# Performance work log

Hardware: AMD Instinct MI355X
Metric: run time of the kernel (lower is better)

The kernel has to match this reference:

```python
import jax, jax.numpy as jnp
import numpy as np

NUM_HEADS = 16


def setup_inputs() -> dict:
    rng = jax.random.key(0)
    ks = jax.random.split(rng, 11)
    T, B, E = 1024, 4, 1024
    s = E ** -0.5  # weight init scale
    return {
        "query": jax.random.normal(ks[0], (T, B, E), jnp.float32),
        "key": jax.random.normal(ks[1], (T, B, E), jnp.float32),
        "value": jax.random.normal(ks[2], (T, B, E), jnp.float32),
        "q_proj_weight": jax.random.normal(ks[3], (E, E), jnp.float32) * s,
        "k_proj_weight1": jax.random.normal(ks[4], (E, E), jnp.float32) * s,
        "k_proj_weight2": jax.random.normal(ks[5], (E, E), jnp.float32) * s,
        "v_proj_weight": jax.random.normal(ks[6], (E, E), jnp.float32) * s,
        "in_proj_bias": jax.random.normal(ks[7], (4 * E,), jnp.float32) * 0.02,
        "out_proj_weight": jax.random.normal(ks[8], (E, E), jnp.float32) * s,
        "out_proj_bias": jax.random.normal(ks[9], (E,), jnp.float32) * 0.02,
        "pi": jax.random.uniform(ks[10], (2, NUM_HEADS), jnp.float32, 0.3, 0.7),
    }


def reference(query, key, value, q_proj_weight, k_proj_weight1, k_proj_weight2,
              v_proj_weight, in_proj_bias, out_proj_weight, out_proj_bias, pi):
    T, Bz, E = query.shape
    H = NUM_HEADS
    hd = E // H
    scaling = hd ** -0.5

    b_q, b_k1, b_k2, b_v = jnp.split(in_proj_bias, 4)
    q = query @ q_proj_weight.T + b_q
    k1 = key @ k_proj_weight1.T + b_k1
    k2 = key @ k_proj_weight2.T + b_k2
    v = value @ v_proj_weight.T + b_v

    def heads(x):  # (S, B, E) -> (B*H, S, hd)
        S = x.shape[0]
        return x.reshape(S, Bz * H, hd).transpose(1, 0, 2)

    q, k1, k2, v = heads(q), heads(k1), heads(k2), heads(v)

    def sqdist(a, b):  # (B*H, Nt, hd), (B*H, Ns, hd) -> (B*H, Nt, Ns)
        a2 = jnp.sum(a * a, axis=-1)
        b2 = jnp.sum(b * b, axis=-1)
        ab = jnp.einsum('btd,bsd->bts', a, b)
        return a2[:, :, None] + b2[:, None, :] - 2.0 * ab

    e1 = jnp.exp(-scaling / 2.0 * sqdist(q, k1))
    e2 = jnp.exp(-3.0 * scaling / 2.0 * sqdist(q, k2))

    pi1 = jnp.clip(jnp.abs(pi[0]), 1e-6, 2.0)  # (H,)
    pi2 = jnp.clip(jnp.abs(pi[1]), 1e-6, 2.0)

    Nt, Ns = e1.shape[1], e1.shape[2]
    attn = (e1.reshape(Bz, H, Nt, Ns) * pi1[None, :, None, None]
            + e2.reshape(Bz, H, Nt, Ns) * pi2[None, :, None, None])
    attn = attn.reshape(Bz * H, Nt, Ns)
    attn = attn / (jnp.sum(attn, axis=-1, keepdims=True) + 1e-6)

    out = jnp.einsum('bts,bsd->btd', attn, v)        # (B*H, Nt, hd)
    out = out.transpose(1, 0, 2).reshape(T, Bz, E)   # (T, B, E)
    return out @ out_proj_weight.T + out_proj_bias
```

## Files before the change

kernel.cpp:

```cpp
#include <hip/hip_runtime.h>
#include <hip/hip_bf16.h>

#define T_DIM 1024
#define B_DIM 4
#define E_DIM 1024
#define H_DIM 16
#define HD    64
#define M_DIM (T_DIM * B_DIM)

typedef __hip_bfloat16 bf16;
typedef __bf16 bf16x8 __attribute__((ext_vector_type(8)));
typedef __bf16 bf16x4 __attribute__((ext_vector_type(4)));
typedef __bf16 bf16x2 __attribute__((ext_vector_type(2)));
typedef float  f32x4  __attribute__((ext_vector_type(4)));

#define P4S ((size_t)M_DIM * E_DIM)
#define P1S ((size_t)E_DIM * E_DIM)

__global__ __launch_bounds__(256) void cvt_all(
    const float* __restrict__ q, const float* __restrict__ k,
    const float* __restrict__ v, const float* __restrict__ w0,
    const float* __restrict__ w1, const float* __restrict__ w2,
    const float* __restrict__ w3, const float* __restrict__ w4,
    __bf16* __restrict__ dst)
{
  size_t i = ((size_t)blockIdx.x * 256 + threadIdx.x) * 8;
  const float* src;
  size_t off;
  if (i < P4S)            { src = q; off = i; }
  else if (i < 2 * P4S)   { src = k; off = i - P4S; }
  else if (i < 3 * P4S)   { src = v; off = i - 2 * P4S; }
  else {
    size_t j = i - 3 * P4S;
    int wsel = (int)(j >> 20);
    off = j & (P1S - 1);
    const float* ws[5] = {w0, w1, w2, w3, w4};
    src = ws[wsel];
  }
  float4 a = *(const float4*)(src + off);
  float4 b = *(const float4*)(src + off + 4);
  bf16x8 o;
  o[0] = (__bf16)a.x; o[1] = (__bf16)a.y; o[2] = (__bf16)a.z; o[3] = (__bf16)a.w;
  o[4] = (__bf16)b.x; o[5] = (__bf16)b.y; o[6] = (__bf16)b.z; o[7] = (__bf16)b.w;
  *(bf16x8*)(dst + i) = o;
}

__device__ __forceinline__ void load_lds16(const __bf16* g, __bf16* l) {
  __builtin_amdgcn_global_load_lds(
      (__attribute__((address_space(1))) void*)(void*)g,
      (__attribute__((address_space(3))) void*)l, 16, 0, 0);
}

__device__ __forceinline__ void stage_half(
    int H, const __bf16* __restrict__ X, const __bf16* __restrict__ W,
    int bm, int bn, __bf16* As, __bf16* Bs, int tid)
{
  if (H >= 64) return;
  const int T  = H >> 2;
  const int h  = H & 3;
  const int rh = (h & 1) * 128;
  const __bf16* src = (h < 2) ? X : W;
  const int rbase   = (h < 2) ? bm : bn;
  __bf16* lb = ((h < 2) ? As : Bs) + (T & 1) * 16384;
#pragma unroll
  for (int li = 0; li < 2; ++li) {
    int r  = rh + li * 64 + (tid >> 3);
    int gc = (tid & 7) ^ (r & 7);
    load_lds16(src + (size_t)(rbase + r) * E_DIM + T * 64 + gc * 8,
               lb + (rh + li * 64) * 64 + tid * 8);
  }
}

#define RD(base, row, c) \
  (*(const bf16x8*)((base) + (row) * 64 + ((((c) ^ ((row) & 7))) << 3)))

__global__ __launch_bounds__(512, 2) void proj_gemm4(
    const __bf16* __restrict__ xbase, const __bf16* __restrict__ wbase,
    const float* __restrict__ bin, __bf16* __restrict__ cbase)
{
  __shared__ __bf16 lds[65536];
  __bf16* As = lds;
  __bf16* Bs = lds + 32768;

  const int z = blockIdx.z;
  const __bf16* X = xbase + ((z == 0) ? 0 : (z == 3) ? 2 * P4S : P4S);
  const __bf16* W = wbase + (size_t)z * P1S;
  const float* bias = bin + z * E_DIM;
  __bf16* C = cbase + (size_t)z * P4S;

  const int bm = blockIdx.x * 256;
  const int bn = blockIdx.y * 256;

  const int tid  = threadIdx.x;
  const int lane = tid & 63;
  const int w    = tid >> 6;
  const int wm   = w >> 2;
  const int wn   = w & 3;
  const int mrow = lane & 15, quad = lane >> 4;

  f32x4 acc[8][4];
#pragma unroll
  for (int m = 0; m < 8; ++m)
#pragma unroll
    for (int n = 0; n < 4; ++n) acc[m][n] = (f32x4)0.0f;

#pragma unroll
  for (int H = 0; H < 5; ++H) stage_half(H, X, W, bm, bn, As, Bs, tid);
  asm volatile("s_waitcnt vmcnt(2)" ::: "memory");
  __builtin_amdgcn_s_barrier();

  bf16x8 af[4][2];
  bf16x8 bq[4][2];

#pragma unroll 2
  for (int t = 0; t < 16; ++t) {
    const __bf16* Ab = As + (t & 1) * 16384;
    const __bf16* Bb = Bs + (t & 1) * 16384;

#pragma unroll
    for (int n = 0; n < 2; ++n)
#pragma unroll
      for (int kk = 0; kk < 2; ++kk)
        bq[n][kk] = RD(Bb, wn * 64 + n * 16 + mrow, kk * 4 + quad);
#pragma unroll
    for (int m = 0; m < 4; ++m)
#pragma unroll
      for (int kk = 0; kk < 2; ++kk)
        af[m][kk] = RD(Ab, wm * 128 + m * 16 + mrow, kk * 4 + quad);
    stage_half(4 * t + 5, X, W, bm, bn, As, Bs, tid);
    __builtin_amdgcn_s_barrier();
    asm volatile("s_waitcnt lgkmcnt(0)" ::: "memory");
    __builtin_amdgcn_s_setprio(1);
#pragma unroll
    for (int kk = 0; kk < 2; ++kk)
#pragma unroll
      for (int n = 0; n < 2; ++n)
#pragma unroll
        for (int m = 0; m < 4; ++m)
          acc[m][n] = __builtin_amdgcn_mfma_f32_16x16x32_bf16(
              af[m][kk], bq[n][kk], acc[m][n], 0, 0, 0);
    __builtin_amdgcn_s_setprio(0);
    __builtin_amdgcn_s_barrier();

#pragma unroll
    for (int n = 2; n < 4; ++n)
#pragma unroll
      for (int kk = 0; kk < 2; ++kk)
        bq[n][kk] = RD(Bb, wn * 64 + n * 16 + mrow, kk * 4 + quad);
    stage_half(4 * t + 6, X, W, bm, bn, As, Bs, tid);
    __builtin_amdgcn_s_barrier();
    asm volatile("s_waitcnt lgkmcnt(0)" ::: "memory");
    __builtin_amdgcn_s_setprio(1);
#pragma unroll
    for (int kk = 0; kk < 2; ++kk)
#pragma unroll
      for (int n = 2; n < 4; ++n)
#pragma unroll
        for (int m = 0; m < 4; ++m)
          acc[m][n] = __builtin_amdgcn_mfma_f32_16x16x32_bf16(
              af[m][kk], bq[n][kk], acc[m][n], 0, 0, 0);
    __builtin_amdgcn_s_setprio(0);
    __builtin_amdgcn_s_barrier();

#pragma unroll
    for (int m = 0; m < 4; ++m)
#pragma unroll
      for (int kk = 0; kk < 2; ++kk)
        af[m][kk] = RD(Ab, wm * 128 + 64 + m * 16 + mrow, kk * 4 + quad);
    stage_half(4 * t + 7, X, W, bm, bn, As, Bs, tid);
    __builtin_amdgcn_s_barrier();
    asm volatile("s_waitcnt lgkmcnt(0)" ::: "memory");
    __builtin_amdgcn_s_setprio(1);
#pragma unroll
    for (int kk = 0; kk < 2; ++kk)
#pragma unroll
      for (int n = 0; n < 2; ++n)
#pragma unroll
        for (int m = 0; m < 4; ++m)
          acc[4 + m][n] = __builtin_amdgcn_mfma_f32_16x16x32_bf16(
              af[m][kk], bq[n][kk], acc[4 + m][n], 0, 0, 0);
    __builtin_amdgcn_s_setprio(0);
    __builtin_amdgcn_s_barrier();

    stage_half(4 * t + 8, X, W, bm, bn, As, Bs, tid);
    __builtin_amdgcn_s_barrier();
    __builtin_amdgcn_s_setprio(1);
#pragma unroll
    for (int kk = 0; kk < 2; ++kk)
#pragma unroll
      for (int n = 2; n < 4; ++n)
#pragma unroll
        for (int m = 0; m < 4; ++m)
          acc[4 + m][n] = __builtin_amdgcn_mfma_f32_16x16x32_bf16(
              af[m][kk], bq[n][kk], acc[4 + m][n], 0, 0, 0);
    __builtin_amdgcn_s_setprio(0);
    if (t < 14)       { asm volatile("s_waitcnt vmcnt(2)" ::: "memory"); }
    else if (t == 14) { asm volatile("s_waitcnt vmcnt(0)" ::: "memory"); }
    __builtin_amdgcn_s_barrier();
  }

#pragma unroll
  for (int n = 0; n < 4; ++n) {
    int col = bn + wn * 64 + n * 16 + mrow;
    float bc = bias[col];
#pragma unroll
    for (int m = 0; m < 8; ++m) {
      int rbase = bm + wm * 128 + m * 16 + quad * 4;
#pragma unroll
      for (int r = 0; r < 4; ++r)
        C[(size_t)(rbase + r) * E_DIM + col] = (__bf16)(acc[m][n][r] + bc);
    }
  }
}

template <typename TO>
__device__ __forceinline__ void gemm_body(
    const __bf16* __restrict__ X, const __bf16* __restrict__ W,
    const float* __restrict__ bias, TO* __restrict__ C,
    int bm, int bn, int Ndim, int Kdim, __bf16* As, __bf16* Bs)
{
  const int tid  = threadIdx.x;
  const int lane = tid & 63;
  const int wave = tid >> 6;
  const int wy = (wave >> 1) * 64;
  const int wx = (wave & 1) * 64;
  const int mrow = lane & 15, quad = lane >> 4;

  const int srow = tid >> 2;
  const int ke   = (tid & 3) * 8;
  const __bf16* gA0 = X + (size_t)(bm + srow)      * Kdim + ke;
  const __bf16* gA1 = X + (size_t)(bm + srow + 64) * Kdim + ke;
  const __bf16* gB0 = W + (size_t)(bn + srow)      * Kdim + ke;
  const __bf16* gB1 = W + (size_t)(bn + srow + 64) * Kdim + ke;
  __bf16* lA0 = As + tid * 8;
  __bf16* lA1 = As + (tid + 256) * 8;
  __bf16* lB0 = Bs + tid * 8;
  __bf16* lB1 = Bs + (tid + 256) * 8;

  f32x4 acc[4][4];
#pragma unroll
  for (int i = 0; i < 4; ++i)
#pragma unroll
    for (int j = 0; j < 4; ++j) acc[i][j] = (f32x4)0.0f;

  for (int k0 = 0; k0 < Kdim; k0 += 32) {
    __syncthreads();
    load_lds16(gA0 + k0, lA0);
    load_lds16(gA1 + k0, lA1);
    load_lds16(gB0 + k0, lB0);
    load_lds16(gB1 + k0, lB1);
    __syncthreads();
    bf16x8 af[4], bf[4];
#pragma unroll
    for (int i = 0; i < 4; ++i)
      af[i] = *(const bf16x8*)(As + (wy + i * 16 + mrow) * 32 + quad * 8);
#pragma unroll
    for (int j = 0; j < 4; ++j)
      bf[j] = *(const bf16x8*)(Bs + (wx + j * 16 + mrow) * 32 + quad * 8);
#pragma unroll
    for (int i = 0; i < 4; ++i)
#pragma unroll
      for (int j = 0; j < 4; ++j)
        acc[i][j] = __builtin_amdgcn_mfma_f32_16x16x32_bf16(af[i], bf[j], acc[i][j], 0, 0, 0);
  }

#pragma unroll
  for (int j = 0; j < 4; ++j) {
    int col = bn + wx + j * 16 + mrow;
    float bc = bias[col];
#pragma unroll
    for (int i = 0; i < 4; ++i) {
      int rbase = bm + wy + i * 16 + quad * 4;
#pragma unroll
      for (int r = 0; r < 4; ++r)
        C[(size_t)(rbase + r) * Ndim + col] = (TO)(acc[i][j][r] + bc);
    }
  }
}

__global__ __launch_bounds__(256) void out_gemm(
    const __bf16* __restrict__ X, const __bf16* __restrict__ W,
    const float* __restrict__ bias, float* __restrict__ C)
{
  __shared__ __bf16 As[128 * 32];
  __shared__ __bf16 Bs[128 * 32];
  gemm_body<float>(X, W, bias, C, blockIdx.x * 128, blockIdx.y * 128,
                   E_DIM, E_DIM, As, Bs);
}

__global__ __launch_bounds__(256) void norms_vt(
    const __bf16* __restrict__ Qp, const __bf16* __restrict__ K1p,
    const __bf16* __restrict__ K2p, const __bf16* __restrict__ Vp,
    float* __restrict__ qn, float* __restrict__ knr,
    __bf16* __restrict__ Vt_g)
{
  __shared__ __bf16 tile[64][88];
  const int tid = threadIdx.x;
  if (blockIdx.x < 768) {
    int id = blockIdx.x * 256 + tid;
    int which = id >> 16;
    int r = id & 65535;
    int bh = r >> 10, t = r & 1023;
    int b = bh >> 4, h = bh & 15;
    const __bf16* src = (which == 0) ? Qp : ((which == 1) ? K1p : K2p);
    const __bf16* p = src + (size_t)(t * 4 + b) * 1024 + h * 64;
    float s = 0.f;
#pragma unroll
    for (int c = 0; c < 8; ++c) {
      bf16x8 v = *(const bf16x8*)(p + c * 8);
#pragma unroll
      for (int j = 0; j < 8; ++j) { float x = (float)v[j]; s += x * x; }
    }
    if (which == 0)
      qn[bh * 1024 + t] = s;
    else
      knr[bh * 2048 + (t >> 5) * 64 + ((which == 2) ? 32 : 0)
          + (t & 15) * 2 + ((t >> 4) & 1)] = s;
    return;
  }
  int bid = blockIdx.x - 768;
  const int bh = bid & 63, kt = bid >> 6;
  const int b = bh >> 4, h = bh & 15;
  {
    int s = tid >> 2, d0 = (tid & 3) * 16;
    const __bf16* src = Vp + (size_t)((kt * 64 + s) * 4 + b) * 1024 + h * 64 + d0;
    *(bf16x8*)(&tile[s][d0])     = *(const bf16x8*)(src);
    *(bf16x8*)(&tile[s][d0 + 8]) = *(const bf16x8*)(src + 8);
  }
  __syncthreads();
#pragma unroll
  for (int c = 0; c < 2; ++c) {
    int idx = tid * 2 + c;
    int d = idx >> 3, u0 = (idx & 7) * 8;
    bf16x8 o;
#pragma unroll
    for (int i = 0; i < 8; ++i) {
      int u = u0 + i;
      int s = (u >> 5) * 32 + ((u & 31) >> 1) + (u & 1) * 16;
      o[i] = tile[s][d];
    }
    *(bf16x8*)(Vt_g + ((size_t)bh * 64 + d) * 1024 + kt * 64 + u0) = o;
  }
}

__global__ __launch_bounds__(256, 2) void mgk_attn_mfma(
    const __bf16* __restrict__ Qp, const __bf16* __restrict__ K1p,
    const __bf16* __restrict__ K2p, const __bf16* __restrict__ Vt_g,
    const float* __restrict__ qn_g, const float* __restrict__ knr_g,
    const float* __restrict__ pi, __bf16* __restrict__ AO)
{
  __shared__ __bf16 lds[20480];
  __bf16* Pl  = lds + 12288;
  float*  knl = (float*)(lds + 16384);

  const int bid = blockIdx.x;
  const int bh  = (bid & 7) * 8 + ((bid >> 3) & 7);
  const int qt  = bid >> 6;
  const int b = bh >> 4, h = bh & 15;
  const int tid = threadIdx.x, lane = tid & 63, w = tid >> 6;
  const int mrow = lane & 15, quad = lane >> 4;

  const float cl1 = 0.0625f * 1.4426950408889634f;
  const float cl2 = 0.1875f * 1.4426950408889634f;
  const float L1 = 2.0f * cl1, L2 = 2.0f * cl2;
  const float p1 = fminf(fmaxf(fabsf(pi[h]), 1e-6f), 2.0f);
  const float p2 = fminf(fmaxf(fabsf(pi[H_DIM + h]), 1e-6f), 2.0f);
  const float lp1 = __log2f(p1), lp2 = __log2f(p2);
  const int hoff = h * 64;

  bf16x8 af[2][2];
  f32x4 aq2[2];
#pragma unroll
  for (int m = 0; m < 2; ++m) {
    const __bf16* qp = Qp + (size_t)((qt * 128 + w * 32 + m * 16 + mrow) * 4 + b) * 1024
                       + hoff + quad * 8;
    af[m][0] = *(const bf16x8*)(qp);
    af[m][1] = *(const bf16x8*)(qp + 32);
    f32x4 qnv = *(const f32x4*)(qn_g + bh * 1024 + qt * 128 + w * 32 + m * 16 + quad * 4);
#pragma unroll
    for (int r = 0; r < 4; ++r) aq2[m][r] = fmaf(cl1 - cl2, qnv[r], lp2);
  }

  bf16x8 onesv;
#pragma unroll
  for (int i = 0; i < 8; ++i) onesv[i] = (__bf16)1.0f;

  const int srow = tid >> 3;
  const int pch  = tid & 7;
  const int gcK  = pch ^ (srow & 7);
  const __bf16* gK1 = K1p + (size_t)(srow * 4 + b) * 1024 + hoff + gcK * 8;
  const __bf16* gK2 = K2p + (size_t)(srow * 4 + b) * 1024 + hoff + gcK * 8;
  const int vcl = pch ^ (srow & 7);
  const int vd  = (vcl >> 2) * 32 + srow;
  const int vu0 = (vcl & 3) * 8;
  const __bf16* gVt = Vt_g + ((size_t)bh * 64 + vd) * 1024 + vu0;

#define STAGE_T(kt_, bsel_) do {                                              \
    __bf16* bb_ = lds + (bsel_) * 6144;                                       \
    load_lds16(gK1 + (size_t)(kt_) * 131072, bb_ + tid * 8);                  \
    load_lds16(gK2 + (size_t)(kt_) * 131072, bb_ + 2048 + tid * 8);           \
    load_lds16(gVt + (kt_) * 32,             bb_ + 4096 + tid * 8);           \
  } while (0)

  load_lds16((const __bf16*)(knr_g + bh * 2048 + tid * 4),
             (__bf16*)knl + tid * 8);
  load_lds16((const __bf16*)(knr_g + bh * 2048 + 1024 + tid * 4),
             (__bf16*)knl + 2048 + tid * 8);
  STAGE_T(0, 0);
  STAGE_T(1, 1);
  asm volatile("s_waitcnt vmcnt(3)" ::: "memory");
  __builtin_amdgcn_s_barrier();

  f32x4 oacc[2][4];
#pragma unroll
  for (int m = 0; m < 2; ++m)
#pragma unroll
    for (int j = 0; j < 4; ++j) oacc[m][j] = (f32x4)0.0f;
  f32x4 osum[2] = {(f32x4)0.0f, (f32x4)0.0f};

  for (int i = 0; i < 32; ++i) {
    const __bf16* buf = lds + (i & 1) * 6144;
    const __bf16* K1s = buf;
    const __bf16* K2s = buf + 2048;
    const __bf16* Vts = buf + 4096;

    float2 f1 = *(const float2*)(knl + i * 64 + mrow * 2);
    float2 f2 = *(const float2*)(knl + i * 64 + 32 + mrow * 2);
    float nb1[2], s2v[2];
    nb1[0] = fmaf(-cl1, f1.x, lp1); nb1[1] = fmaf(-cl1, f1.y, lp1);
    s2v[0] = -cl2 * f2.x;           s2v[1] = -cl2 * f2.y;

    f32x4 acc1[2][2], acc2[2][2];
#pragma unroll
    for (int m = 0; m < 2; ++m)
#pragma unroll
      for (int j = 0; j < 2; ++j) { acc1[m][j] = (f32x4)0.0f; acc2[m][j] = (f32x4)0.0f; }
    __builtin_amdgcn_s_setprio(1);
#pragma unroll
    for (int kk = 0; kk < 2; ++kk)
#pragma unroll
      for (int j = 0; j < 2; ++j) {
        int row = j * 16 + mrow;
        int off = row * 64 + (((kk * 4 + quad) ^ (row & 7)) << 3);
        bf16x8 b1f = *(const bf16x8*)(K1s + off);
        bf16x8 b2f = *(const bf16x8*)(K2s + off);
#pragma unroll
        for (int m = 0; m < 2; ++m) {
          acc1[m][j] = __builtin_amdgcn_mfma_f32_16x16x32_bf16(af[m][kk], b1f, acc1[m][j], 0, 0, 0);
          acc2[m][j] = __builtin_amdgcn_mfma_f32_16x16x32_bf16(af[m][kk], b2f, acc2[m][j], 0, 0, 0);
        }
      }
    __builtin_amdgcn_s_setprio(0);

#pragma unroll
    for (int m = 0; m < 2; ++m) {
      f32x4 pj[2];
#pragma unroll
      for (int j = 0; j < 2; ++j) {
        f32x4 p;
#pragma unroll
        for (int r = 0; r < 4; ++r) {
          float e1 = __builtin_amdgcn_exp2f(fmaf(L1, acc1[m][j][r], nb1[j]));
          float e2 = __builtin_amdgcn_exp2f(fmaf(L2, acc2[m][j][r], s2v[j] + aq2[m][r]));
          p[r] = e1 + e2;
        }
        pj[j] = p;
      }
#pragma unroll
      for (int r = 0; r < 4; ++r) {
        int row  = quad * 4 + r;
        int phys = (m * 4 + (mrow >> 2)) ^ (row & 7);
        bf16x2 pk; pk[0] = (__bf16)pj[0][r]; pk[1] = (__bf16)pj[1][r];
        *(bf16x2*)(Pl + w * 1024 + row * 64 + phys * 8 + (mrow & 3) * 2) = pk;
      }
    }

    bf16x8 pf[2];
#pragma unroll
    for (int m = 0; m < 2; ++m)
      pf[m] = *(const bf16x8*)(Pl + w * 1024 + mrow * 64
                               + (((m * 4 + quad) ^ (mrow & 7)) << 3));
    __builtin_amdgcn_s_setprio(1);
#pragma unroll
    for (int m = 0; m < 2; ++m)
      osum[m] = __builtin_amdgcn_mfma_f32_16x16x32_bf16(pf[m], onesv, osum[m], 0, 0, 0);
#pragma unroll
    for (int j = 0; j < 4; ++j) {
      int rowv = (j & 1) * 16 + mrow;
      int cl   = (j >> 1) * 4 + quad;
      bf16x8 vf = *(const bf16x8*)(Vts + rowv * 64 + ((cl ^ (rowv & 7)) << 3));
#pragma unroll
      for (int m = 0; m < 2; ++m)
        oacc[m][j] = __builtin_amdgcn_mfma_f32_16x16x32_bf16(pf[m], vf, oacc[m][j], 0, 0, 0);
    }
    __builtin_amdgcn_s_setprio(0);

    if (i < 31) {
      asm volatile("s_waitcnt lgkmcnt(0)" ::: "memory");
      __builtin_amdgcn_s_barrier();
      if (i < 30) {
        STAGE_T(i + 2, i & 1);
        asm volatile("s_waitcnt vmcnt(3)" ::: "memory");
      } else {
        asm volatile("s_waitcnt vmcnt(0)" ::: "memory");
      }
      __builtin_amdgcn_s_barrier();
    }
  }
#undef STAGE_T

#pragma unroll
  for (int m = 0; m < 2; ++m) {
    f32x4 inv;
#pragma unroll
    for (int r = 0; r < 4; ++r) inv[r] = 1.0f / (osum[m][r] + 1e-6f);
#pragma unroll
    for (int j = 0; j < 4; ++j) {
      int col = hoff + j * 16 + mrow;
#pragma unroll
      for (int r = 0; r < 4; ++r) {
        int t = qt * 128 + w * 32 + m * 16 + quad * 4 + r;
        AO[(size_t)(t * 4 + b) * 1024 + col] = (__bf16)(oacc[m][j][r] * inv[r]);
      }
    }
  }
}

extern "C" void kernel_launch(void* const* d_in, const int* in_sizes, int n_in,
                              void* d_out, int out_size, void* d_ws, size_t ws_size,
                              hipStream_t stream) {
  const float* query = (const float*)d_in[0];
  const float* key   = (const float*)d_in[1];
  const float* value = (const float*)d_in[2];
  const float* Wq    = (const float*)d_in[3];
  const float* Wk1   = (const float*)d_in[4];
  const float* Wk2   = (const float*)d_in[5];
  const float* Wv    = (const float*)d_in[6];
  const float* bin   = (const float*)d_in[7];
  const float* Wo    = (const float*)d_in[8];
  const float* bo    = (const float*)d_in[9];
  const float* pi    = (const float*)d_in[10];
  float* out = (float*)d_out;

  __bf16* qc  = (__bf16*)d_ws;
  __bf16* wq  = qc  + 3 * P4S;
  __bf16* wo  = wq  + 4 * P1S;
  __bf16* Qp  = wq  + 5 * P1S;
  __bf16* K1p = Qp  + P4S;
  __bf16* K2p = K1p + P4S;
  __bf16* Vp  = K2p + P4S;
  __bf16* AO  = Vp  + P4S;
  float*  qn_g = (float*)(AO + P4S);
  float*  knr  = qn_g + 64 * 1024;
  __bf16* Vt_g = qc;

  cvt_all<<<8704, 256, 0, stream>>>(query, key, value, Wq, Wk1, Wk2, Wv, Wo, qc);

  proj_gemm4<<<dim3(M_DIM / 256, E_DIM / 256, 4), 512, 0, stream>>>(qc, wq, bin, Qp);

  norms_vt<<<768 + 1024, 256, 0, stream>>>(Qp, K1p, K2p, Vp,
                                           qn_g, knr, Vt_g);

  mgk_attn_mfma<<<512, 256, 0, stream>>>(
      Qp, K1p, K2p, Vt_g, qn_g, knr, pi, AO);

  out_gemm<<<dim3(M_DIM / 128, E_DIM / 128), 256, 0, stream>>>(AO, wo, bo, out);
}
```

Before: 238.8 us.

## Swap MFMA operands so P stays in registers, drop LDS round-trip and ones-MFMA

```diff
diff --git a/kernel.cpp b/kernel.cpp
--- a/kernel.cpp
+++ b/kernel.cpp
@@ -314,8 +314,7 @@
     if (which == 0)
       qn[bh * 1024 + t] = s;
     else
-      knr[bh * 2048 + (t >> 5) * 64 + ((which == 2) ? 32 : 0)
-          + (t & 15) * 2 + ((t >> 4) & 1)] = s;
+      knr[bh * 2048 + (t >> 5) * 64 + ((which == 2) ? 32 : 0) + (t & 31)] = s;
     return;
   }
   int bid = blockIdx.x - 768;
@@ -336,7 +335,8 @@
 #pragma unroll
     for (int i = 0; i < 8; ++i) {
       int u = u0 + i;
-      int s = (u >> 5) * 32 + ((u & 31) >> 1) + (u & 1) * 16;
+      int u32 = u & 31;
+      int s = (u >> 5) * 32 + ((u32 >> 2) & 1) * 16 + (u32 >> 3) * 4 + (u32 & 3);
       o[i] = tile[s][d];
     }
     *(bf16x8*)(Vt_g + ((size_t)bh * 64 + d) * 1024 + kt * 64 + u0) = o;
@@ -349,9 +349,8 @@
     const float* __restrict__ qn_g, const float* __restrict__ knr_g,
     const float* __restrict__ pi, __bf16* __restrict__ AO)
 {
-  __shared__ __bf16 lds[20480];
-  __bf16* Pl  = lds + 12288;
-  float*  knl = (float*)(lds + 16384);
+  __shared__ __bf16 lds[16384];
+  float*  knl = (float*)(lds + 12288);
 
   const int bid = blockIdx.x;
   const int bh  = (bid & 7) * 8 + ((bid >> 3) & 7);
@@ -369,21 +368,16 @@
   const int hoff = h * 64;
 
   bf16x8 af[2][2];
-  f32x4 aq2[2];
+  float aq2s[2];
 #pragma unroll
   for (int m = 0; m < 2; ++m) {
     const __bf16* qp = Qp + (size_t)((qt * 128 + w * 32 + m * 16 + mrow) * 4 + b) * 1024
                        + hoff + quad * 8;
     af[m][0] = *(const bf16x8*)(qp);
     af[m][1] = *(const bf16x8*)(qp + 32);
-    f32x4 qnv = *(const f32x4*)(qn_g + bh * 1024 + qt * 128 + w * 32 + m * 16 + quad * 4);
-#pragma unroll
-    for (int r = 0; r < 4; ++r) aq2[m][r] = fmaf(cl1 - cl2, qnv[r], lp2);
-  }
-
-  bf16x8 onesv;
-#pragma unroll
-  for (int i = 0; i < 8; ++i) onesv[i] = (__bf16)1.0f;
+    aq2s[m] = fmaf(cl1 - cl2,
+                   qn_g[bh * 1024 + qt * 128 + w * 32 + m * 16 + mrow], lp2);
+  }
 
   const int srow = tid >> 3;
   const int pch  = tid & 7;
@@ -416,7 +410,7 @@
   for (int m = 0; m < 2; ++m)
 #pragma unroll
     for (int j = 0; j < 4; ++j) oacc[m][j] = (f32x4)0.0f;
-  f32x4 osum[2] = {(f32x4)0.0f, (f32x4)0.0f};
+  float rs[2] = {0.0f, 0.0f};
 
   for (int i = 0; i < 32; ++i) {
     const __bf16* buf = lds + (i & 1) * 6144;
@@ -424,17 +418,18 @@
     const __bf16* K2s = buf + 2048;
     const __bf16* Vts = buf + 4096;
 
-    float2 f1 = *(const float2*)(knl + i * 64 + mrow * 2);
-    float2 f2 = *(const float2*)(knl + i * 64 + 32 + mrow * 2);
-    float nb1[2], s2v[2];
-    nb1[0] = fmaf(-cl1, f1.x, lp1); nb1[1] = fmaf(-cl1, f1.y, lp1);
-    s2v[0] = -cl2 * f2.x;           s2v[1] = -cl2 * f2.y;
-
-    f32x4 acc1[2][2], acc2[2][2];
+    const float* knt = knl + i * 64;
+    f32x4 kn1j[2], kn2j[2];
+    kn1j[0] = *(const f32x4*)(knt + quad * 4);
+    kn1j[1] = *(const f32x4*)(knt + 16 + quad * 4);
+    kn2j[0] = *(const f32x4*)(knt + 32 + quad * 4);
+    kn2j[1] = *(const f32x4*)(knt + 48 + quad * 4);
+
+    f32x4 a1[2][2], a2[2][2];
 #pragma unroll
     for (int m = 0; m < 2; ++m)
 #pragma unroll
-      for (int j = 0; j < 2; ++j) { acc1[m][j] = (f32x4)0.0f; acc2[m][j] = (f32x4)0.0f; }
+      for (int j = 0; j < 2; ++j) { a1[m][j] = (f32x4)0.0f; a2[m][j] = (f32x4)0.0f; }
     __builtin_amdgcn_s_setprio(1);
 #pragma unroll
     for (int kk = 0; kk < 2; ++kk)
@@ -446,44 +441,35 @@
         bf16x8 b2f = *(const bf16x8*)(K2s + off);
 #pragma unroll
         for (int m = 0; m < 2; ++m) {
-          acc1[m][j] = __builtin_amdgcn_mfma_f32_16x16x32_bf16(af[m][kk], b1f, acc1[m][j], 0, 0, 0);
-          acc2[m][j] = __builtin_amdgcn_mfma_f32_16x16x32_bf16(af[m][kk], b2f, acc2[m][j], 0, 0, 0);
+          a1[m][j] = __builtin_amdgcn_mfma_f32_16x16x32_bf16(b1f, af[m][kk], a1[m][j], 0, 0, 0);
+          a2[m][j] = __builtin_amdgcn_mfma_f32_16x16x32_bf16(b2f, af[m][kk], a2[m][j], 0, 0, 0);
         }
       }
     __builtin_amdgcn_s_setprio(0);
 
+    bf16x8 pf[2];
 #pragma unroll
     for (int m = 0; m < 2; ++m) {
-      f32x4 pj[2];
 #pragma unroll
       for (int j = 0; j < 2; ++j) {
         f32x4 p;
 #pragma unroll
         for (int r = 0; r < 4; ++r) {
-          float e1 = __builtin_amdgcn_exp2f(fmaf(L1, acc1[m][j][r], nb1[j]));
-          float e2 = __builtin_amdgcn_exp2f(fmaf(L2, acc2[m][j][r], s2v[j] + aq2[m][r]));
+          float e1 = __builtin_amdgcn_exp2f(
+              fmaf(L1, a1[m][j][r], fmaf(-cl1, kn1j[j][r], lp1)));
+          float e2 = __builtin_amdgcn_exp2f(
+              fmaf(L2, a2[m][j][r], fmaf(-cl2, kn2j[j][r], aq2s[m])));
           p[r] = e1 + e2;
         }
-        pj[j] = p;
+        rs[m] += (p[0] + p[1]) + (p[2] + p[3]);
+        pf[m][j * 4 + 0] = (__bf16)p[0];
+        pf[m][j * 4 + 1] = (__bf16)p[1];
+        pf[m][j * 4 + 2] = (__bf16)p[2];
+        pf[m][j * 4 + 3] = (__bf16)p[3];
       }
-#pragma unroll
-      for (int r = 0; r < 4; ++r) {
-        int row  = quad * 4 + r;
-        int phys = (m * 4 + (mrow >> 2)) ^ (row & 7);
-        bf16x2 pk; pk[0] = (__bf16)pj[0][r]; pk[1] = (__bf16)pj[1][r];
-        *(bf16x2*)(Pl + w * 1024 + row * 64 + phys * 8 + (mrow & 3) * 2) = pk;
-      }
-    }
-
-    bf16x8 pf[2];
-#pragma unroll
-    for (int m = 0; m < 2; ++m)
-      pf[m] = *(const bf16x8*)(Pl + w * 1024 + mrow * 64
-                               + (((m * 4 + quad) ^ (mrow & 7)) << 3));
+    }
+
     __builtin_amdgcn_s_setprio(1);
-#pragma unroll
-    for (int m = 0; m < 2; ++m)
-      osum[m] = __builtin_amdgcn_mfma_f32_16x16x32_bf16(pf[m], onesv, osum[m], 0, 0, 0);
 #pragma unroll
     for (int j = 0; j < 4; ++j) {
       int rowv = (j & 1) * 16 + mrow;
@@ -509,11 +495,20 @@
   }
 #undef STAGE_T
 
+  float rst[2];
+#pragma unroll
+  for (int m = 0; m < 2; ++m) {
+    float v = rs[m];
+    v += __shfl_xor(v, 16, 64);
+    v += __shfl_xor(v, 32, 64);
+    rst[m] = v;
+  }
 #pragma unroll
   for (int m = 0; m < 2; ++m) {
     f32x4 inv;
 #pragma unroll
-    for (int r = 0; r < 4; ++r) inv[r] = 1.0f / (osum[m][r] + 1e-6f);
+    for (int r = 0; r < 4; ++r)
+      inv[r] = 1.0f / (__shfl(rst[m], quad * 4 + r, 64) + 1e-6f);
 #pragma unroll
     for (int j = 0; j < 4; ++j) {
       int col = hoff + j * 16 + mrow;
```

After: 240.6 us. About the same (+0.8%).
